# Performance work log

Measured on AMD Instinct MI355X. Metric: run time of the kernel, lower is better.

## Reference

```python
import jax, jax.numpy as jnp
import numpy as np

B, N, DIN, DOUT, H = 4, 2048, 512, 512, 8
HD = DOUT // H


def setup_inputs() -> dict:
    key = jax.random.key(0)
    ks = jax.random.split(key, 8)
    x = jax.random.normal(ks[0], (B, N, DIN), dtype=jnp.float32)
    mask = jax.random.randint(ks[1], (B, 1, N, N), 0, 2, dtype=jnp.int32)
    s = 1.0 / np.sqrt(DIN)
    Wq = jax.random.uniform(ks[2], (DOUT, DIN), jnp.float32, -s, s)
    Wk = jax.random.uniform(ks[3], (DOUT, DIN), jnp.float32, -s, s)
    Wv = jax.random.uniform(ks[4], (DOUT, DIN), jnp.float32, -s, s)
    bq = jax.random.uniform(ks[5], (DOUT,), jnp.float32, -s, s)
    bk = jax.random.uniform(ks[6], (DOUT,), jnp.float32, -s, s)
    bv = jax.random.uniform(ks[7], (DOUT,), jnp.float32, -s, s)
    return {"x": x, "Wq": Wq, "bq": bq, "Wk": Wk, "bk": bk, "Wv": Wv, "bv": bv, "mask": mask}


def reference(x, Wq, bq, Wk, bk, Wv, bv, mask):
    b, n, _ = x.shape
    # torch Linear: y = x @ W.T + b ; split heads -> [b, h, n, hd]
    def proj(W, bias):
        y = jnp.einsum('bnd,od->bno', x, W) + bias
        return y.reshape(b, n, H, HD).transpose(0, 2, 1, 3)
    Q, K, V = proj(Wq, bq), proj(Wk, bk), proj(Wv, bv)
    scores = jnp.einsum('bhnd,bhmd->bhnm', Q, K) / np.sqrt(HD).astype(np.float32)
    scores = jnp.where(mask == 0, jnp.float32(-1e9), scores)
    attn = jax.nn.softmax(scores, axis=-1)
    ctx = jnp.einsum('bhnm,bhmd->bhnd', attn, V)
    ctx = ctx.transpose(0, 2, 1, 3).reshape(b, n, DOUT)
    return jax.nn.elu(ctx)
```

## Files before the change

kernel.cpp:

```cpp
#include <hip/hip_runtime.h>
#include <math.h>
#include <stdint.h>

#define CB 4
#define CN 2048
#define CDIN 512
#define CDOUT 512
#define CH 8
#define CHD 64
#define CM (CB * CN)
#define CBH (CB * CH)
#define NKT (CN / 64)

typedef _Float16 f16x8 __attribute__((ext_vector_type(8)));
typedef _Float16 f16x4 __attribute__((ext_vector_type(4)));
typedef float    f32x4 __attribute__((ext_vector_type(4)));

#define QSCALE 0.1803368801111204f

#define PB_X  2048
#define PB_WQ 2176
#define PB_WK 2304
#define PB_WV 2432
#define PB_MB 3456

__global__ __launch_bounds__(256) void prep_kernel(
    const float* __restrict__ x,  _Float16* __restrict__ xh,
    const float* __restrict__ Wq, _Float16* __restrict__ wqh,
    const float* __restrict__ Wk, _Float16* __restrict__ wkh,
    const float* __restrict__ Wv, _Float16* __restrict__ wvh,
    const int* __restrict__ mask, unsigned long long* __restrict__ mbits)
{
    const int bx = blockIdx.x;
    if (bx >= PB_WV) {
        const int lane = threadIdx.x & 63;
        const int wv   = threadIdx.x >> 6;
        const int wbase = (bx - PB_WV) * 256 + wv * 64;
        unsigned long long myword = 0;
        #pragma unroll 8
        for (int it = 0; it < 64; ++it) {
            int v = mask[(size_t)(wbase + it) * 64 + lane];
            unsigned long long bal = __ballot(v != 0);
            if (lane == it) myword = bal;
        }
        mbits[wbase + lane] = myword;
        return;
    }
    const float* s; _Float16* d; int i;
    if (bx < PB_X)       { s = x;  d = xh;  i = bx * 2048 + threadIdx.x * 8; }
    else if (bx < PB_WQ) { s = Wq; d = wqh; i = (bx - PB_X)  * 2048 + threadIdx.x * 8; }
    else if (bx < PB_WK) { s = Wk; d = wkh; i = (bx - PB_WQ) * 2048 + threadIdx.x * 8; }
    else                 { s = Wv; d = wvh; i = (bx - PB_WK) * 2048 + threadIdx.x * 8; }
    float4 a = *(const float4*)&s[i];
    float4 b = *(const float4*)&s[i + 4];
    f16x8 h = {(_Float16)a.x, (_Float16)a.y, (_Float16)a.z, (_Float16)a.w,
               (_Float16)b.x, (_Float16)b.y, (_Float16)b.z, (_Float16)b.w};
    *(f16x8*)&d[i] = h;
}

__global__ __launch_bounds__(256) void proj_kernel(
    const _Float16* __restrict__ xh,
    const _Float16* __restrict__ Wqh, const float* __restrict__ bq,
    const _Float16* __restrict__ Wkh, const float* __restrict__ bk,
    const _Float16* __restrict__ Wvh, const float* __restrict__ bv,
    _Float16* __restrict__ Qf, _Float16* __restrict__ Kf, _Float16* __restrict__ Vt)
{
    const int z = blockIdx.z;
    const _Float16* W; const float* bias;
    if (z == 0)      { W = Wqh; bias = bq; }
    else if (z == 1) { W = Wkh; bias = bk; }
    else             { W = Wvh; bias = bv; }

    __shared__ _Float16 SM[2 * 128 * 72];

    const int tid  = threadIdx.x;
    const int m0   = blockIdx.x * 128;
    const int o0   = blockIdx.y * 128;
    const int lane = tid & 63, w = tid >> 6;
    const int il   = lane & 15, quad = lane >> 4;
    const int srow = tid >> 3, kc = (tid & 7) * 8;

    f32x4 acc[2][8] = {};
    f16x8 xr[4], wr[4];

    #pragma unroll
    for (int i = 0; i < 4; ++i) {
        xr[i] = *(const f16x8*)&xh[(size_t)(m0 + srow + i * 32) * CDIN + kc];
        wr[i] = *(const f16x8*)&W[(size_t)(o0 + srow + i * 32) * CDIN + kc];
    }

    for (int k0 = 0; k0 < CDIN; k0 += 64) {
        #pragma unroll
        for (int i = 0; i < 4; ++i) {
            *(f16x8*)&SM[(srow + i * 32) * 72 + kc] = xr[i];
            *(f16x8*)&SM[9216 + (srow + i * 32) * 72 + kc] = wr[i];
        }
        __syncthreads();

        if (k0 + 64 < CDIN) {
            #pragma unroll
            for (int i = 0; i < 4; ++i) {
                xr[i] = *(const f16x8*)&xh[(size_t)(m0 + srow + i * 32) * CDIN + k0 + 64 + kc];
                wr[i] = *(const f16x8*)&W[(size_t)(o0 + srow + i * 32) * CDIN + k0 + 64 + kc];
            }
        }

        #pragma unroll
        for (int dh = 0; dh < 2; ++dh) {
            f16x8 X0 = *(const f16x8*)&SM[(w * 32 + il) * 72 + dh * 32 + quad * 8];
            f16x8 X1 = *(const f16x8*)&SM[(w * 32 + 16 + il) * 72 + dh * 32 + quad * 8];
            if (z < 2) {
                #pragma unroll
                for (int s = 0; s < 8; ++s) {
                    f16x8 Wv_ = *(const f16x8*)&SM[9216 + (s * 16 + il) * 72 + dh * 32 + quad * 8];
                    acc[0][s] = __builtin_amdgcn_mfma_f32_16x16x32_f16(Wv_, X0, acc[0][s], 0, 0, 0);
                    acc[1][s] = __builtin_amdgcn_mfma_f32_16x16x32_f16(Wv_, X1, acc[1][s], 0, 0, 0);
                }
            } else {
                #pragma unroll
                for (int s = 0; s < 8; ++s) {
                    f16x8 Wv_ = *(const f16x8*)&SM[9216 + (s * 16 + il) * 72 + dh * 32 + quad * 8];
                    acc[0][s] = __builtin_amdgcn_mfma_f32_16x16x32_f16(X0, Wv_, acc[0][s], 0, 0, 0);
                    acc[1][s] = __builtin_amdgcn_mfma_f32_16x16x32_f16(X1, Wv_, acc[1][s], 0, 0, 0);
                }
            }
        }
        __syncthreads();
    }

    const int b  = m0 / CN;
    const int nb = m0 & (CN - 1);
    if (z < 2) {
        const float sc = (z == 0) ? QSCALE : 1.0f;
        #pragma unroll
        for (int s = 0; s < 8; ++s) {
            #pragma unroll
            for (int mi = 0; mi < 2; ++mi) {
                f16x4 pv;
                #pragma unroll
                for (int r = 0; r < 4; ++r)
                    pv[r] = (_Float16)((acc[mi][s][r] + bias[o0 + s * 16 + quad * 4 + r]) * sc);
                *(f16x4*)&SM[(w * 32 + mi * 16 + il) * 140 + s * 16 + quad * 4] = pv;
            }
        }
    } else {
        #pragma unroll
        for (int s = 0; s < 8; ++s) {
            const float bval = bias[o0 + s * 16 + il];
            #pragma unroll
            for (int mi = 0; mi < 2; ++mi) {
                f16x4 pv = {(_Float16)(acc[mi][s][0] + bval),
                            (_Float16)(acc[mi][s][1] + bval),
                            (_Float16)(acc[mi][s][2] + bval),
                            (_Float16)(acc[mi][s][3] + bval)};
                *(f16x4*)&SM[(s * 16 + il) * 140 + w * 32 + mi * 16 + quad * 4] = pv;
            }
        }
    }
    __syncthreads();

    const int uu   = tid & 127;
    const int hseg = tid >> 7;
    const int bh   = b * CH + (o0 >> 6) + hseg;
    if (z < 2) {
        _Float16* dst = ((z == 0) ? Qf : Kf) + ((size_t)bh * CN + nb) * CHD;
        #pragma unroll
        for (int k = 0; k < 8; ++k) {
            int n = k * 16 + (uu >> 3);
            int d = (uu & 7) * 8;
            *(f16x8*)&dst[(size_t)n * CHD + d] =
                *(const f16x8*)&SM[n * 140 + hseg * 64 + d];
        }
    } else {
        _Float16* dst = Vt + (size_t)bh * CHD * CN + nb;
        #pragma unroll
        for (int k = 0; k < 8; ++k) {
            int d = k * 8 + (uu >> 4);
            int n = (uu & 15) * 8;
            *(f16x8*)&dst[(size_t)d * CN + n] =
                *(const f16x8*)&SM[(hseg * 64 + d) * 140 + n];
        }
    }
}

__global__ __launch_bounds__(256) void attn_kernel(
    const _Float16* __restrict__ Qf, const _Float16* __restrict__ Kf,
    const _Float16* __restrict__ Vt, const unsigned long long* __restrict__ mbits,
    float* __restrict__ out)
{
    __shared__ uint4 Ks4[2][64][8];
    __shared__ uint4 Vs4[2][64][8];
    __shared__ uint4 Ps4[4][32][8];

    const int tid  = threadIdx.x;
    const int q0   = blockIdx.x * 128;
    const int bh   = blockIdx.y;
    const int b    = bh >> 3, h = bh & 7;
    const int lane = tid & 63, w = tid >> 6;
    const int il   = lane & 15, quad = lane >> 4;
    const int i7   = il & 7;

    const int srow = tid >> 2;
    const int sg   = (tid & 3) * 2;
    const int sw0  = sg       ^ (srow & 7);
    const int sw1  = (sg + 1) ^ (srow & 7);

    _Float16* Pw = (_Float16*)&Ps4[w][0][0];

    const _Float16* Qb = Qf + (size_t)bh * CN * CHD;
    const _Float16* Kb = Kf + (size_t)bh * CN * CHD;
    const _Float16* Vb = Vt + (size_t)bh * CHD * CN;

    const int qg0 = q0 + w * 32 + il;
    const int qg1 = qg0 + 16;
    const unsigned long long* mrow0 = mbits + ((size_t)b * CN + qg0) * NKT;
    const unsigned long long* mrow1 = mbits + ((size_t)b * CN + qg1) * NKT;

    f16x8 Qa[2][2];
    Qa[0][0] = *(const f16x8*)&Qb[(size_t)qg0 * CHD + quad * 8];
    Qa[0][1] = *(const f16x8*)&Qb[(size_t)qg0 * CHD + 32 + quad * 8];
    Qa[1][0] = *(const f16x8*)&Qb[(size_t)qg1 * CHD + quad * 8];
    Qa[1][1] = *(const f16x8*)&Qb[(size_t)qg1 * CHD + 32 + quad * 8];

    const f16x8 ones = {1.f16, 1.f16, 1.f16, 1.f16, 1.f16, 1.f16, 1.f16, 1.f16};

    f32x4 oacc[2][4] = {};
    f32x4 lacc[2] = {};

    uint4 kA0, kA1, vA0, vA1;
    unsigned long long mn0, mn1;
    kA0 = *(const uint4*)&Kb[(size_t)srow * CHD + sg * 8];
    kA1 = *(const uint4*)&Kb[(size_t)srow * CHD + sg * 8 + 8];
    vA0 = *(const uint4*)&Vb[(size_t)srow * CN + sg * 8];
    vA1 = *(const uint4*)&Vb[(size_t)srow * CN + sg * 8 + 8];
    mn0 = mrow0[0];
    mn1 = mrow1[0];
    Ks4[0][srow][sw0] = kA0; Ks4[0][srow][sw1] = kA1;
    Vs4[0][srow][sw0] = vA0; Vs4[0][srow][sw1] = vA1;
    __syncthreads();

    for (int kt = 0; kt < NKT; ++kt) {
        const int cur = kt & 1;
        const unsigned long long mc0 = mn0, mc1 = mn1;

        if (kt < NKT - 1) {
            const size_t ko = (size_t)((kt + 1) * 64 + srow) * CHD + sg * 8;
            kA0 = *(const uint4*)&Kb[ko];
            kA1 = *(const uint4*)&Kb[ko + 8];
            const size_t vo = (size_t)srow * CN + (kt + 1) * 64 + sg * 8;
            vA0 = *(const uint4*)&Vb[vo];
            vA1 = *(const uint4*)&Vb[vo + 8];
            mn0 = mrow0[kt + 1];
            mn1 = mrow1[kt + 1];
        }

        f32x4 st[2][4] = {};
        #pragma unroll
        for (int s = 0; s < 4; ++s) {
            f16x8 A0 = *(const f16x8*)&Ks4[cur][s * 16 + il][quad ^ i7];
            f16x8 A1 = *(const f16x8*)&Ks4[cur][s * 16 + il][(4 + quad) ^ i7];
            st[0][s] = __builtin_amdgcn_mfma_f32_16x16x32_f16(A0, Qa[0][0], st[0][s], 0, 0, 0);
            st[0][s] = __builtin_amdgcn_mfma_f32_16x16x32_f16(A1, Qa[0][1], st[0][s], 0, 0, 0);
            st[1][s] = __builtin_amdgcn_mfma_f32_16x16x32_f16(A0, Qa[1][0], st[1][s], 0, 0, 0);
            st[1][s] = __builtin_amdgcn_mfma_f32_16x16x32_f16(A1, Qa[1][1], st[1][s], 0, 0, 0);
        }

        #pragma unroll
        for (int g = 0; g < 2; ++g) {
            const unsigned long long mw = g ? mc1 : mc0;
            const uint32_t mlo = (uint32_t)mw, mhi = (uint32_t)(mw >> 32);
            #pragma unroll
            for (int s = 0; s < 4; ++s) {
                const uint32_t mm = (s < 2) ? mlo : mhi;
                const int base = ((s & 1) << 4) + quad * 4;
                f16x4 pv;
                #pragma unroll
                for (int r = 0; r < 4; ++r) {
                    float sv = ((mm >> (base + r)) & 1u) ? st[g][s][r] : -1e9f;
                    pv[r] = (_Float16)__builtin_amdgcn_exp2f(sv);
                }
                const int pg = (s * 2 + (quad >> 1)) ^ i7;
                *(f16x4*)&Pw[(g * 16 + il) * 64 + pg * 8 + (quad & 1) * 4] = pv;
            }
        }

        f16x8 Pa[2][2];
        #pragma unroll
        for (int g = 0; g < 2; ++g) {
            Pa[g][0] = *(const f16x8*)&Pw[(g * 16 + il) * 64 + (quad ^ i7) * 8];
            Pa[g][1] = *(const f16x8*)&Pw[(g * 16 + il) * 64 + ((4 + quad) ^ i7) * 8];
        }
        #pragma unroll
        for (int s = 0; s < 4; ++s) {
            f16x8 B0 = *(const f16x8*)&Vs4[cur][s * 16 + il][quad ^ i7];
            f16x8 B1 = *(const f16x8*)&Vs4[cur][s * 16 + il][(4 + quad) ^ i7];
            oacc[0][s] = __builtin_amdgcn_mfma_f32_16x16x32_f16(Pa[0][0], B0, oacc[0][s], 0, 0, 0);
            oacc[0][s] = __builtin_amdgcn_mfma_f32_16x16x32_f16(Pa[0][1], B1, oacc[0][s], 0, 0, 0);
            oacc[1][s] = __builtin_amdgcn_mfma_f32_16x16x32_f16(Pa[1][0], B0, oacc[1][s], 0, 0, 0);
            oacc[1][s] = __builtin_amdgcn_mfma_f32_16x16x32_f16(Pa[1][1], B1, oacc[1][s], 0, 0, 0);
        }
        lacc[0] = __builtin_amdgcn_mfma_f32_16x16x32_f16(Pa[0][0], ones, lacc[0], 0, 0, 0);
        lacc[0] = __builtin_amdgcn_mfma_f32_16x16x32_f16(Pa[0][1], ones, lacc[0], 0, 0, 0);
        lacc[1] = __builtin_amdgcn_mfma_f32_16x16x32_f16(Pa[1][0], ones, lacc[1], 0, 0, 0);
        lacc[1] = __builtin_amdgcn_mfma_f32_16x16x32_f16(Pa[1][1], ones, lacc[1], 0, 0, 0);

        if (kt < NKT - 1) {
            const int nxt = cur ^ 1;
            Ks4[nxt][srow][sw0] = kA0; Ks4[nxt][srow][sw1] = kA1;
            Vs4[nxt][srow][sw0] = vA0; Vs4[nxt][srow][sw1] = vA1;
            __syncthreads();
        }
    }

    #pragma unroll
    for (int g = 0; g < 2; ++g) {
        #pragma unroll
        for (int s = 0; s < 4; ++s) {
            const int d = h * CHD + s * 16 + il;
            #pragma unroll
            for (int r = 0; r < 4; ++r) {
                int n = q0 + w * 32 + g * 16 + quad * 4 + r;
                float c = oacc[g][s][r] / lacc[g][r];
                out[((size_t)b * CN + n) * CDOUT + d] = c > 0.f ? c : expm1f(c);
            }
        }
    }
}

extern "C" void kernel_launch(void* const* d_in, const int* in_sizes, int n_in,
                              void* d_out, int out_size, void* d_ws, size_t ws_size,
                              hipStream_t stream) {
    const float* x    = (const float*)d_in[0];
    const float* Wq   = (const float*)d_in[1];
    const float* bq   = (const float*)d_in[2];
    const float* Wk   = (const float*)d_in[3];
    const float* bk   = (const float*)d_in[4];
    const float* Wv   = (const float*)d_in[5];
    const float* bv   = (const float*)d_in[6];
    const int*   mask = (const int*)d_in[7];
    float* out = (float*)d_out;

    const size_t nx = (size_t)CM * CDIN;
    const size_t nw = (size_t)CDOUT * CDIN;
    const size_t nt = (size_t)CBH * CN * CHD;
    _Float16* xh  = (_Float16*)d_ws;
    _Float16* wqh = xh + nx;
    _Float16* wkh = wqh + nw;
    _Float16* wvh = wkh + nw;
    _Float16* Qf  = wvh + nw;
    _Float16* Kf  = Qf + nt;
    _Float16* Vt  = Kf + nt;
    unsigned long long* mbits = (unsigned long long*)(Vt + nt);

    prep_kernel<<<dim3(PB_MB), 256, 0, stream>>>(
        x, xh, Wq, wqh, Wk, wkh, Wv, wvh, mask, mbits);
    proj_kernel<<<dim3(CM / 128, CDOUT / 128, 3), 256, 0, stream>>>(
        xh, wqh, bq, wkh, bk, wvh, bv, Qf, Kf, Vt);
    attn_kernel<<<dim3(CN / 128, CBH), 256, 0, stream>>>(
        Qf, Kf, Vt, mbits, out);
}
```

Baseline: 217.7 us.

## Split attention key range across two wave groups with LDS reduction

The attention block grows to 512 threads. Two groups of four waves each process half of the key sequence for the same 128 queries, and their partial output and row-sum accumulators are combined through shared memory at the end. The aim is more waves per block and a shorter serial key loop per wave, to hide latency. In exchange, the double-buffered K/V prefetch is replaced by a single buffer per group, which needs two block-wide barriers per iteration, and the reduction and write phase at the end adds extra work.

```diff
diff --git a/kernel.cpp b/kernel.cpp
--- a/kernel.cpp
+++ b/kernel.cpp
@@ -183,27 +183,32 @@
     }
 }
 
-__global__ __launch_bounds__(256) void attn_kernel(
+__global__ __launch_bounds__(512, 4) void attn_kernel(
     const _Float16* __restrict__ Qf, const _Float16* __restrict__ Kf,
     const _Float16* __restrict__ Vt, const unsigned long long* __restrict__ mbits,
     float* __restrict__ out)
 {
     __shared__ uint4 Ks4[2][64][8];
     __shared__ uint4 Vs4[2][64][8];
-    __shared__ uint4 Ps4[4][32][8];
+    __shared__ uint4 Ps4[8][32][8];
 
     const int tid  = threadIdx.x;
     const int q0   = blockIdx.x * 128;
     const int bh   = blockIdx.y;
     const int b    = bh >> 3, h = bh & 7;
     const int lane = tid & 63, w = tid >> 6;
+    const int kg   = w >> 2;
+    const int wi   = w & 3;
     const int il   = lane & 15, quad = lane >> 4;
     const int i7   = il & 7;
 
-    const int srow = tid >> 2;
-    const int sg   = (tid & 3) * 2;
+    const int gtid = tid & 255;
+    const int srow = gtid >> 2;
+    const int sg   = (gtid & 3) * 2;
     const int sw0  = sg       ^ (srow & 7);
     const int sw1  = (sg + 1) ^ (srow & 7);
+
+    const int kb = kg * 1024;
 
     _Float16* Pw = (_Float16*)&Ps4[w][0][0];
 
@@ -211,10 +216,10 @@
     const _Float16* Kb = Kf + (size_t)bh * CN * CHD;
     const _Float16* Vb = Vt + (size_t)bh * CHD * CN;
 
-    const int qg0 = q0 + w * 32 + il;
+    const int qg0 = q0 + wi * 32 + il;
     const int qg1 = qg0 + 16;
-    const unsigned long long* mrow0 = mbits + ((size_t)b * CN + qg0) * NKT;
-    const unsigned long long* mrow1 = mbits + ((size_t)b * CN + qg1) * NKT;
+    const unsigned long long* mrow0 = mbits + ((size_t)b * CN + qg0) * NKT + kg * 16;
+    const unsigned long long* mrow1 = mbits + ((size_t)b * CN + qg1) * NKT + kg * 16;
 
     f16x8 Qa[2][2];
     Qa[0][0] = *(const f16x8*)&Qb[(size_t)qg0 * CHD + quad * 8];
@@ -229,36 +234,35 @@
 
     uint4 kA0, kA1, vA0, vA1;
     unsigned long long mn0, mn1;
-    kA0 = *(const uint4*)&Kb[(size_t)srow * CHD + sg * 8];
-    kA1 = *(const uint4*)&Kb[(size_t)srow * CHD + sg * 8 + 8];
-    vA0 = *(const uint4*)&Vb[(size_t)srow * CN + sg * 8];
-    vA1 = *(const uint4*)&Vb[(size_t)srow * CN + sg * 8 + 8];
+    kA0 = *(const uint4*)&Kb[(size_t)(kb + srow) * CHD + sg * 8];
+    kA1 = *(const uint4*)&Kb[(size_t)(kb + srow) * CHD + sg * 8 + 8];
+    vA0 = *(const uint4*)&Vb[(size_t)srow * CN + kb + sg * 8];
+    vA1 = *(const uint4*)&Vb[(size_t)srow * CN + kb + sg * 8 + 8];
     mn0 = mrow0[0];
     mn1 = mrow1[0];
-    Ks4[0][srow][sw0] = kA0; Ks4[0][srow][sw1] = kA1;
-    Vs4[0][srow][sw0] = vA0; Vs4[0][srow][sw1] = vA1;
+    Ks4[kg][srow][sw0] = kA0; Ks4[kg][srow][sw1] = kA1;
+    Vs4[kg][srow][sw0] = vA0; Vs4[kg][srow][sw1] = vA1;
     __syncthreads();
 
-    for (int kt = 0; kt < NKT; ++kt) {
-        const int cur = kt & 1;
+    for (int t = 0; t < 16; ++t) {
         const unsigned long long mc0 = mn0, mc1 = mn1;
 
-        if (kt < NKT - 1) {
-            const size_t ko = (size_t)((kt + 1) * 64 + srow) * CHD + sg * 8;
+        if (t < 15) {
+            const size_t ko = (size_t)(kb + (t + 1) * 64 + srow) * CHD + sg * 8;
             kA0 = *(const uint4*)&Kb[ko];
             kA1 = *(const uint4*)&Kb[ko + 8];
-            const size_t vo = (size_t)srow * CN + (kt + 1) * 64 + sg * 8;
+            const size_t vo = (size_t)srow * CN + kb + (t + 1) * 64 + sg * 8;
             vA0 = *(const uint4*)&Vb[vo];
             vA1 = *(const uint4*)&Vb[vo + 8];
-            mn0 = mrow0[kt + 1];
-            mn1 = mrow1[kt + 1];
+            mn0 = mrow0[t + 1];
+            mn1 = mrow1[t + 1];
         }
 
         f32x4 st[2][4] = {};
         #pragma unroll
         for (int s = 0; s < 4; ++s) {
-            f16x8 A0 = *(const f16x8*)&Ks4[cur][s * 16 + il][quad ^ i7];
-            f16x8 A1 = *(const f16x8*)&Ks4[cur][s * 16 + il][(4 + quad) ^ i7];
+            f16x8 A0 = *(const f16x8*)&Ks4[kg][s * 16 + il][quad ^ i7];
+            f16x8 A1 = *(const f16x8*)&Ks4[kg][s * 16 + il][(4 + quad) ^ i7];
             st[0][s] = __builtin_amdgcn_mfma_f32_16x16x32_f16(A0, Qa[0][0], st[0][s], 0, 0, 0);
             st[0][s] = __builtin_amdgcn_mfma_f32_16x16x32_f16(A1, Qa[0][1], st[0][s], 0, 0, 0);
             st[1][s] = __builtin_amdgcn_mfma_f32_16x16x32_f16(A0, Qa[1][0], st[1][s], 0, 0, 0);
@@ -292,8 +296,8 @@
         }
         #pragma unroll
         for (int s = 0; s < 4; ++s) {
-            f16x8 B0 = *(const f16x8*)&Vs4[cur][s * 16 + il][quad ^ i7];
-            f16x8 B1 = *(const f16x8*)&Vs4[cur][s * 16 + il][(4 + quad) ^ i7];
+            f16x8 B0 = *(const f16x8*)&Vs4[kg][s * 16 + il][quad ^ i7];
+            f16x8 B1 = *(const f16x8*)&Vs4[kg][s * 16 + il][(4 + quad) ^ i7];
             oacc[0][s] = __builtin_amdgcn_mfma_f32_16x16x32_f16(Pa[0][0], B0, oacc[0][s], 0, 0, 0);
             oacc[0][s] = __builtin_amdgcn_mfma_f32_16x16x32_f16(Pa[0][1], B1, oacc[0][s], 0, 0, 0);
             oacc[1][s] = __builtin_amdgcn_mfma_f32_16x16x32_f16(Pa[1][0], B0, oacc[1][s], 0, 0, 0);
@@ -304,24 +308,49 @@
         lacc[1] = __builtin_amdgcn_mfma_f32_16x16x32_f16(Pa[1][0], ones, lacc[1], 0, 0, 0);
         lacc[1] = __builtin_amdgcn_mfma_f32_16x16x32_f16(Pa[1][1], ones, lacc[1], 0, 0, 0);
 
-        if (kt < NKT - 1) {
-            const int nxt = cur ^ 1;
-            Ks4[nxt][srow][sw0] = kA0; Ks4[nxt][srow][sw1] = kA1;
-            Vs4[nxt][srow][sw0] = vA0; Vs4[nxt][srow][sw1] = vA1;
+        if (t < 15) {
             __syncthreads();
-        }
-    }
-
-    #pragma unroll
-    for (int g = 0; g < 2; ++g) {
-        #pragma unroll
-        for (int s = 0; s < 4; ++s) {
-            const int d = h * CHD + s * 16 + il;
-            #pragma unroll
-            for (int r = 0; r < 4; ++r) {
-                int n = q0 + w * 32 + g * 16 + quad * 4 + r;
-                float c = oacc[g][s][r] / lacc[g][r];
-                out[((size_t)b * CN + n) * CDOUT + d] = c > 0.f ? c : expm1f(c);
+            Ks4[kg][srow][sw0] = kA0; Ks4[kg][srow][sw1] = kA1;
+            Vs4[kg][srow][sw0] = vA0; Vs4[kg][srow][sw1] = vA1;
+            __syncthreads();
+        }
+    }
+
+    __syncthreads();
+    f32x4* Ob = (f32x4*)&Ps4[0][0][0];
+    f32x4* Lb = (f32x4*)&Ks4[0][0][0];
+    const int obase = (wi * 64 + lane) * 8;
+    const int lbase = (wi * 64 + lane) * 2;
+    if (kg == 1) {
+        #pragma unroll
+        for (int g = 0; g < 2; ++g)
+            #pragma unroll
+            for (int s = 0; s < 4; ++s)
+                Ob[obase + ((g * 4 + s) ^ (lane & 7))] = oacc[g][s];
+        Lb[lbase + (lane & 1)]       = lacc[0];
+        Lb[lbase + ((lane & 1) ^ 1)] = lacc[1];
+    }
+    __syncthreads();
+    if (kg == 0) {
+        lacc[0] += Lb[lbase + (lane & 1)];
+        lacc[1] += Lb[lbase + ((lane & 1) ^ 1)];
+        #pragma unroll
+        for (int g = 0; g < 2; ++g)
+            #pragma unroll
+            for (int s = 0; s < 4; ++s)
+                oacc[g][s] += Ob[obase + ((g * 4 + s) ^ (lane & 7))];
+
+        #pragma unroll
+        for (int g = 0; g < 2; ++g) {
+            #pragma unroll
+            for (int s = 0; s < 4; ++s) {
+                const int d = h * CHD + s * 16 + il;
+                #pragma unroll
+                for (int r = 0; r < 4; ++r) {
+                    int n = q0 + wi * 32 + g * 16 + quad * 4 + r;
+                    float c = oacc[g][s][r] / lacc[g][r];
+                    out[((size_t)b * CN + n) * CDOUT + d] = c > 0.f ? c : expm1f(c);
+                }
             }
         }
     }
@@ -356,6 +385,6 @@
         x, xh, Wq, wqh, Wk, wkh, Wv, wvh, mask, mbits);
     proj_kernel<<<dim3(CM / 128, CDOUT / 128, 3), 256, 0, stream>>>(
         xh, wqh, bq, wkh, bk, wvh, bv, Qf, Kf, Vt);
-    attn_kernel<<<dim3(CN / 128, CBH), 256, 0, stream>>>(
+    attn_kernel<<<dim3(CN / 128, CBH), 512, 0, stream>>>(
         Qf, Kf, Vt, mbits, out);
 }
```

New measurement: 216.0 us. No clear change (-0.8%).
